# Kernel tuning notes

Measured on AMD Instinct MI355X. Metric: run time of the kernel, lower is better.

Reference implementation:

```python
import jax, jax.numpy as jnp
import numpy as np

BATCH, HIDDEN, NUM_SEEDS, CHUNK, NUM_BLUEPRINTS = 8192, 4096, 32, 128, 10


def setup_inputs() -> dict:
    key = jax.random.key(0)
    ks = jax.random.split(key, 6)
    x = jax.random.normal(ks[0], (BATCH, HIDDEN), dtype=jnp.float32)
    lifecycle_states = jax.random.randint(ks[1], (NUM_SEEDS,), 0, 8, dtype=jnp.int32)
    blueprint_ids = jax.random.randint(ks[2], (NUM_SEEDS,), 0, NUM_BLUEPRINTS, dtype=jnp.int32)
    grafting_strategies = jax.random.randint(ks[3], (NUM_SEEDS,), 0, 3, dtype=jnp.int32)
    blend_factors = jax.random.uniform(ks[4], (NUM_SEEDS,), dtype=jnp.float32)
    blueprint_weights = jax.random.normal(ks[5], (NUM_BLUEPRINTS, HIDDEN), dtype=jnp.float32)
    return {
        "x": x,
        "lifecycle_states": lifecycle_states,
        "blueprint_ids": blueprint_ids,
        "grafting_strategies": grafting_strategies,
        "blend_factors": blend_factors,
        "blueprint_weights": blueprint_weights,
    }


def reference(x, lifecycle_states, blueprint_ids, grafting_strategies, blend_factors, blueprint_weights):
    B, H = x.shape
    S = lifecycle_states.shape[0]
    C = H // S  # chunk_size; hidden_dim = num_seeds * chunk_size
    xc = x.reshape(B, S, C)  # [B, S, C] per-seed chunks

    # Per-seed gather of the blueprint weight chunk:
    # w[s, c] = blueprint_weights[blueprint_ids[s], s*C + c]
    flat_w = blueprint_weights.reshape(-1)
    base = blueprint_ids * H + jnp.arange(S, dtype=jnp.int32) * C  # [S]
    w = flat_w[base[:, None] + jnp.arange(C, dtype=jnp.int32)[None, :]]  # [S, C]

    active = (lifecycle_states >= 3) & (lifecycle_states <= 6)  # [S]
    alpha = blend_factors[None, :, None]  # [1, S, 1]
    wb = w[None, :, :]  # [1, S, C]

    blend0 = alpha * wb * xc + (1.0 - alpha) * xc  # grafting_strategy == 0
    blend1 = wb * xc                               # grafting_strategy == 1
    blend2 = xc + wb                               # else
    strat = grafting_strategies[None, :, None]
    blended = jnp.where(strat == 0, blend0, jnp.where(strat == 1, blend1, blend2))

    out = jnp.where(active[None, :, None], blended, xc).reshape(B, H)

    # Fused telemetry over raw activations, per seed (buffers zeroed each call)
    tsum = xc.sum(axis=(0, 2))                 # [S]
    tsumsq = (xc * xc).sum(axis=(0, 2))        # [S]
    tcount = jnp.full((S,), float(B * C), dtype=jnp.float32)
    return out, tsum, tsumsq, tcount
```

## Files before the change

kernel.cpp:

```cpp
#include <hip/hip_runtime.h>

namespace {

constexpr int kBatch  = 8192;
constexpr int kHidden = 4096;
constexpr int kSeeds  = 32;
constexpr int kChunk  = 128;
constexpr int kTpb    = 256;

typedef float fvec4 __attribute__((ext_vector_type(4)));

__global__ __launch_bounds__(kTpb) void kasmina_main(
    const float* __restrict__ x,
    const int*   __restrict__ life,
    const int*   __restrict__ bid,
    const int*   __restrict__ strat,
    const float* __restrict__ alpha,
    const float* __restrict__ bw,
    float*       __restrict__ out,
    float*       __restrict__ psum,
    float*       __restrict__ psumsq)
{
    const int t  = threadIdx.x;
    const int c0 = (t & 31) * 4;

    fvec4 mcoef[4];
    fvec4 acoef[4];
    float ssum[4];
    float ssq[4];

    #pragma unroll
    for (int j = 0; j < 4; ++j) {
        const int   s   = (t >> 5) + j * 8;
        const int   lf  = life[s];
        const bool  act = (lf >= 3) && (lf <= 6);
        const int   st  = strat[s];
        const float al  = alpha[s];
        const fvec4 w = *reinterpret_cast<const fvec4*>(
            &bw[bid[s] * kHidden + s * kChunk + c0]);

        fvec4 mm = {1.f, 1.f, 1.f, 1.f};
        fvec4 aa = {0.f, 0.f, 0.f, 0.f};
        if (act) {
            if (st == 0) {
                const float om = 1.f - al;
                mm = al * w + om;
            } else if (st == 1) {
                mm = w;
            } else {
                aa = w;
            }
        }
        mcoef[j] = mm;
        acoef[j] = aa;
        ssum[j]  = 0.f;
        ssq[j]   = 0.f;
    }

    for (int r = blockIdx.x; r < kBatch; r += gridDim.x) {
        const fvec4* __restrict__ xrow =
            reinterpret_cast<const fvec4*>(x + (size_t)r * kHidden);
        fvec4* __restrict__ orow =
            reinterpret_cast<fvec4*>(out + (size_t)r * kHidden);
        #pragma unroll
        for (int j = 0; j < 4; ++j) {
            const int idx = t + j * kTpb;
            const fvec4 xv = xrow[idx];
            fvec4 ov;
            ov.x = fmaf(mcoef[j].x, xv.x, acoef[j].x);
            ov.y = fmaf(mcoef[j].y, xv.y, acoef[j].y);
            ov.z = fmaf(mcoef[j].z, xv.z, acoef[j].z);
            ov.w = fmaf(mcoef[j].w, xv.w, acoef[j].w);
            __builtin_nontemporal_store(ov, &orow[idx]);
            ssum[j] += (xv.x + xv.y) + (xv.z + xv.w);
            ssq[j]  = fmaf(xv.x, xv.x, ssq[j]);
            ssq[j]  = fmaf(xv.y, xv.y, ssq[j]);
            ssq[j]  = fmaf(xv.z, xv.z, ssq[j]);
            ssq[j]  = fmaf(xv.w, xv.w, ssq[j]);
        }
    }

    #pragma unroll
    for (int j = 0; j < 4; ++j) {
        float a = ssum[j];
        float b = ssq[j];
        #pragma unroll
        for (int off = 1; off < 32; off <<= 1) {
            a += __shfl_xor(a, off, 64);
            b += __shfl_xor(b, off, 64);
        }
        if ((t & 31) == 0) {
            const int s = (t >> 5) + j * 8;
            psum[blockIdx.x * kSeeds + s]   = a;
            psumsq[blockIdx.x * kSeeds + s] = b;
        }
    }
}

__global__ __launch_bounds__(kTpb) void kasmina_reduce(
    const float* __restrict__ psum,
    const float* __restrict__ psumsq,
    float*       __restrict__ tail,
    int nblk)
{
    const int s = blockIdx.x;
    const int t = threadIdx.x;
    float a = 0.f, b = 0.f;
    for (int blk = t; blk < nblk; blk += kTpb) {
        a += psum[(size_t)blk * kSeeds + s];
        b += psumsq[(size_t)blk * kSeeds + s];
    }
    #pragma unroll
    for (int off = 1; off < 64; off <<= 1) {
        a += __shfl_xor(a, off, 64);
        b += __shfl_xor(b, off, 64);
    }
    __shared__ float la[4], lb[4];
    if ((t & 63) == 0) { la[t >> 6] = a; lb[t >> 6] = b; }
    __syncthreads();
    if (t == 0) {
        a = (la[0] + la[1]) + (la[2] + la[3]);
        b = (lb[0] + lb[1]) + (lb[2] + lb[3]);
        tail[s]              = a;
        tail[kSeeds + s]     = b;
        tail[2 * kSeeds + s] = (float)(kBatch * kChunk);
    }
}

}

extern "C" void kernel_launch(void* const* d_in, const int* in_sizes, int n_in,
                              void* d_out, int out_size, void* d_ws, size_t ws_size,
                              hipStream_t stream) {
    const float* x     = (const float*)d_in[0];
    const int*   life  = (const int*)d_in[1];
    const int*   bid   = (const int*)d_in[2];
    const int*   strat = (const int*)d_in[3];
    const float* alpha = (const float*)d_in[4];
    const float* bw    = (const float*)d_in[5];
    float*       out   = (float*)d_out;

    int nblk = 2048;
    const size_t per_blk = (size_t)kSeeds * 2 * sizeof(float);
    if ((size_t)nblk * per_blk > ws_size) {
        nblk = (int)(ws_size / per_blk);
        if (nblk < 1) nblk = 1;
    }
    float* psum   = (float*)d_ws;
    float* psumsq = psum + (size_t)nblk * kSeeds;

    kasmina_main<<<nblk, kTpb, 0, stream>>>(x, life, bid, strat, alpha, bw,
                                            out, psum, psumsq);

    float* tail = out + (size_t)kBatch * kHidden;
    kasmina_reduce<<<kSeeds, kTpb, 0, stream>>>(psum, psumsq, tail, nblk);
}
```

Before: 53.06 us.

## Use 1024-thread blocks covering full rows with contiguous row ranges per block

Each block now has 1024 threads, so every thread owns a fixed 4-column slice of a single seed. Each of 512 blocks processes a contiguous range of 16 rows, with four row loads issued before compute. This cuts per-thread coefficient and accumulator registers and enlarges the memory-level parallelism per iteration. The partial-sum layout becomes seed-major so the final reduce reads contiguously with one wavefront per seed. The cost is fewer blocks (512) and large blocks that may limit occupancy flexibility. The ws_size guard was dropped, so it assumes the workspace is large enough.

```diff
diff --git a/kernel.cpp b/kernel.cpp
--- a/kernel.cpp
+++ b/kernel.cpp
@@ -6,7 +6,9 @@
 constexpr int kHidden = 4096;
 constexpr int kSeeds  = 32;
 constexpr int kChunk  = 128;
-constexpr int kTpb    = 256;
+constexpr int kTpb    = 1024;
+constexpr int kBlocks = 512;
+constexpr int kRowsPerBlk = kBatch / kBlocks;
 
 typedef float fvec4 __attribute__((ext_vector_type(4)));
 
@@ -22,82 +24,71 @@
     float*       __restrict__ psumsq)
 {
     const int t  = threadIdx.x;
+    const int s  = t >> 5;
     const int c0 = (t & 31) * 4;
 
-    fvec4 mcoef[4];
-    fvec4 acoef[4];
-    float ssum[4];
-    float ssq[4];
+    const int   lf  = life[s];
+    const bool  act = (lf >= 3) && (lf <= 6);
+    const int   st  = strat[s];
+    const float al  = alpha[s];
+    const fvec4 w   = *reinterpret_cast<const fvec4*>(
+        &bw[bid[s] * kHidden + s * kChunk + c0]);
+
+    fvec4 mm = {1.f, 1.f, 1.f, 1.f};
+    fvec4 aa = {0.f, 0.f, 0.f, 0.f};
+    if (act) {
+        if (st == 0) {
+            mm = al * w + (1.f - al);
+        } else if (st == 1) {
+            mm = w;
+        } else {
+            aa = w;
+        }
+    }
+
+    float ssum = 0.f;
+    float ssq  = 0.f;
+
+    const int r0 = blockIdx.x * kRowsPerBlk;
+    const float* __restrict__ xbase = x   + (size_t)r0 * kHidden + 4 * t;
+    float*       __restrict__ obase = out + (size_t)r0 * kHidden + 4 * t;
 
     #pragma unroll
-    for (int j = 0; j < 4; ++j) {
-        const int   s   = (t >> 5) + j * 8;
-        const int   lf  = life[s];
-        const bool  act = (lf >= 3) && (lf <= 6);
-        const int   st  = strat[s];
-        const float al  = alpha[s];
-        const fvec4 w = *reinterpret_cast<const fvec4*>(
-            &bw[bid[s] * kHidden + s * kChunk + c0]);
-
-        fvec4 mm = {1.f, 1.f, 1.f, 1.f};
-        fvec4 aa = {0.f, 0.f, 0.f, 0.f};
-        if (act) {
-            if (st == 0) {
-                const float om = 1.f - al;
-                mm = al * w + om;
-            } else if (st == 1) {
-                mm = w;
-            } else {
-                aa = w;
-            }
-        }
-        mcoef[j] = mm;
-        acoef[j] = aa;
-        ssum[j]  = 0.f;
-        ssq[j]   = 0.f;
-    }
-
-    for (int r = blockIdx.x; r < kBatch; r += gridDim.x) {
-        const fvec4* __restrict__ xrow =
-            reinterpret_cast<const fvec4*>(x + (size_t)r * kHidden);
-        fvec4* __restrict__ orow =
-            reinterpret_cast<fvec4*>(out + (size_t)r * kHidden);
+    for (int rc = 0; rc < kRowsPerBlk; rc += 4) {
+        fvec4 xv[4];
         #pragma unroll
-        for (int j = 0; j < 4; ++j) {
-            const int idx = t + j * kTpb;
-            const fvec4 xv = xrow[idx];
+        for (int k = 0; k < 4; ++k)
+            xv[k] = *reinterpret_cast<const fvec4*>(
+                xbase + (size_t)(rc + k) * kHidden);
+        #pragma unroll
+        for (int k = 0; k < 4; ++k) {
             fvec4 ov;
-            ov.x = fmaf(mcoef[j].x, xv.x, acoef[j].x);
-            ov.y = fmaf(mcoef[j].y, xv.y, acoef[j].y);
-            ov.z = fmaf(mcoef[j].z, xv.z, acoef[j].z);
-            ov.w = fmaf(mcoef[j].w, xv.w, acoef[j].w);
-            __builtin_nontemporal_store(ov, &orow[idx]);
-            ssum[j] += (xv.x + xv.y) + (xv.z + xv.w);
-            ssq[j]  = fmaf(xv.x, xv.x, ssq[j]);
-            ssq[j]  = fmaf(xv.y, xv.y, ssq[j]);
-            ssq[j]  = fmaf(xv.z, xv.z, ssq[j]);
-            ssq[j]  = fmaf(xv.w, xv.w, ssq[j]);
+            ov.x = fmaf(mm.x, xv[k].x, aa.x);
+            ov.y = fmaf(mm.y, xv[k].y, aa.y);
+            ov.z = fmaf(mm.z, xv[k].z, aa.z);
+            ov.w = fmaf(mm.w, xv[k].w, aa.w);
+            __builtin_nontemporal_store(
+                ov, reinterpret_cast<fvec4*>(obase + (size_t)(rc + k) * kHidden));
+            ssum += (xv[k].x + xv[k].y) + (xv[k].z + xv[k].w);
+            ssq   = fmaf(xv[k].x, xv[k].x, ssq);
+            ssq   = fmaf(xv[k].y, xv[k].y, ssq);
+            ssq   = fmaf(xv[k].z, xv[k].z, ssq);
+            ssq   = fmaf(xv[k].w, xv[k].w, ssq);
         }
     }
 
     #pragma unroll
-    for (int j = 0; j < 4; ++j) {
-        float a = ssum[j];
-        float b = ssq[j];
-        #pragma unroll
-        for (int off = 1; off < 32; off <<= 1) {
-            a += __shfl_xor(a, off, 64);
-            b += __shfl_xor(b, off, 64);
-        }
-        if ((t & 31) == 0) {
-            const int s = (t >> 5) + j * 8;
-            psum[blockIdx.x * kSeeds + s]   = a;
-            psumsq[blockIdx.x * kSeeds + s] = b;
-        }
+    for (int off = 1; off < 32; off <<= 1) {
+        ssum += __shfl_xor(ssum, off, 64);
+        ssq  += __shfl_xor(ssq,  off, 64);
+    }
+    if ((t & 31) == 0) {
+        psum[s * kBlocks + blockIdx.x]   = ssum;
+        psumsq[s * kBlocks + blockIdx.x] = ssq;
     }
 }
 
-__global__ __launch_bounds__(kTpb) void kasmina_reduce(
+__global__ __launch_bounds__(64) void kasmina_reduce(
     const float* __restrict__ psum,
     const float* __restrict__ psumsq,
     float*       __restrict__ tail,
@@ -106,21 +97,16 @@
     const int s = blockIdx.x;
     const int t = threadIdx.x;
     float a = 0.f, b = 0.f;
-    for (int blk = t; blk < nblk; blk += kTpb) {
-        a += psum[(size_t)blk * kSeeds + s];
-        b += psumsq[(size_t)blk * kSeeds + s];
+    for (int i = t; i < nblk; i += 64) {
+        a += psum[(size_t)s * nblk + i];
+        b += psumsq[(size_t)s * nblk + i];
     }
     #pragma unroll
     for (int off = 1; off < 64; off <<= 1) {
         a += __shfl_xor(a, off, 64);
         b += __shfl_xor(b, off, 64);
     }
-    __shared__ float la[4], lb[4];
-    if ((t & 63) == 0) { la[t >> 6] = a; lb[t >> 6] = b; }
-    __syncthreads();
     if (t == 0) {
-        a = (la[0] + la[1]) + (la[2] + la[3]);
-        b = (lb[0] + lb[1]) + (lb[2] + lb[3]);
         tail[s]              = a;
         tail[kSeeds + s]     = b;
         tail[2 * kSeeds + s] = (float)(kBatch * kChunk);
@@ -140,18 +126,12 @@
     const float* bw    = (const float*)d_in[5];
     float*       out   = (float*)d_out;
 
-    int nblk = 2048;
-    const size_t per_blk = (size_t)kSeeds * 2 * sizeof(float);
-    if ((size_t)nblk * per_blk > ws_size) {
-        nblk = (int)(ws_size / per_blk);
-        if (nblk < 1) nblk = 1;
-    }
     float* psum   = (float*)d_ws;
-    float* psumsq = psum + (size_t)nblk * kSeeds;
+    float* psumsq = psum + (size_t)kSeeds * kBlocks;
 
-    kasmina_main<<<nblk, kTpb, 0, stream>>>(x, life, bid, strat, alpha, bw,
-                                            out, psum, psumsq);
+    kasmina_main<<<kBlocks, kTpb, 0, stream>>>(x, life, bid, strat, alpha, bw,
+                                               out, psum, psumsq);
 
     float* tail = out + (size_t)kBatch * kHidden;
-    kasmina_reduce<<<kSeeds, kTpb, 0, stream>>>(psum, psumsq, tail, nblk);
+    kasmina_reduce<<<kSeeds, 64, 0, stream>>>(psum, psumsq, tail, kBlocks);
 }
```

After: 49.54 us. -6.6%, faster.
